# Kernel tuning notes

Hardware: AMD Instinct MI355X
Metric: run time of the kernel (lower is better)

The kernel has to match this reference:

```python
import jax, jax.numpy as jnp
import numpy as np

N_LOC, N_EVT, E = 100000, 200000, 1000000
F_LOC, F_EVT, H = 128, 128, 64


def setup_inputs() -> dict:
    key = jax.random.key(0)
    ks = jax.random.split(key, 12)
    s = lambda k, shp: jax.random.normal(k, shp, dtype=jnp.float32) * (1.0 / np.sqrt(shp[0]))
    return {
        "loc_x": jax.random.normal(ks[0], (N_LOC, F_LOC), dtype=jnp.float32),
        "evt_x": jax.random.normal(ks[1], (N_EVT, F_EVT), dtype=jnp.float32),
        "edge_index": jax.random.randint(ks[2], (2, E), 0, N_LOC, dtype=jnp.int64),
        # projections (stored as (in, out))
        "W_loc": s(ks[3], (F_LOC, H)), "b_loc": jnp.zeros((H,), jnp.float32),
        "W_evt": s(ks[4], (F_EVT, H)), "b_evt": jnp.zeros((H,), jnp.float32),
        # SAGEConv: lin_l (on aggregated src, with bias), lin_r (on dst root, no bias)
        "W_l": s(ks[5], (H, H)), "b_l": jnp.zeros((H,), jnp.float32),
        "W_r": s(ks[6], (H, H)),
        # head MLP
        "W_h1": s(ks[7], (H, H // 2)), "b_h1": jnp.zeros((H // 2,), jnp.float32),
        "W_h2": s(ks[8], (H // 2, 1)), "b_h2": jnp.zeros((1,), jnp.float32),
    }


def reference(loc_x, evt_x, edge_index, W_loc, b_loc, W_evt, b_evt,
              W_l, b_l, W_r, W_h1, b_h1, W_h2, b_h2):
    # node projections + ReLU
    loc_h = jax.nn.relu(loc_x @ W_loc + b_loc)   # [N_loc, H]
    evt_h = jax.nn.relu(evt_x @ W_evt + b_evt)   # [N_evt, H]

    src, dst = edge_index[0], edge_index[1]      # event -> location
    n_loc = loc_h.shape[0]
    # mean aggregation of source (event) features onto destination (location) nodes
    msg_sum = jax.ops.segment_sum(evt_h[src], dst, num_segments=n_loc)   # [N_loc, H]
    cnt = jax.ops.segment_sum(jnp.ones_like(dst, dtype=loc_h.dtype), dst,
                              num_segments=n_loc)
    agg = msg_sum / jnp.maximum(cnt, 1.0)[:, None]
    # SAGEConv: lin_l(agg) + lin_r(root), then ReLU
    loc_h = jax.nn.relu(agg @ W_l + b_l + loc_h @ W_r)

    # prediction head
    h = jax.nn.relu(loc_h @ W_h1 + b_h1)
    logits = (h @ W_h2 + b_h2)[:, 0]             # [N_loc]
    return logits
```

## Files before the change

### kernel.cpp

```cpp
#include <hip/hip_runtime.h>


#define N_LOC 100000
#define N_EVT 200000
#define E_CNT 1000000
#define NTILES 6250
#define NBKT   256
#define BKT_L  391
#define CAPG   6000
#define QCAP   32
#define BKT_BLK 512
#define PERB   1954

#define PROJ_EVT_BLK 512
#define PROJ_LOC_BLK 256
#define PROJ_BLK_TOT (PROJ_EVT_BLK + PROJ_LOC_BLK)
#define EVT_TILES 12500
#define LOC_TILES 6250
#define HEAD_BLK  512

typedef __attribute__((ext_vector_type(8))) short short8;
typedef __attribute__((ext_vector_type(4))) float floatx4;

__device__ __forceinline__ float b2f(unsigned short u) {
    unsigned int x = ((unsigned int)u) << 16;
    return __builtin_bit_cast(float, x);
}
__device__ __forceinline__ unsigned short f2b(float f) {
    unsigned int x = __builtin_bit_cast(unsigned int, f);
    unsigned int r = (x + 0x7fffu + ((x >> 16) & 1u)) >> 16;
    return (unsigned short)r;
}
__device__ __forceinline__ float loadf(const void* p, int f32, size_t i) {
    return f32 ? ((const float*)p)[i] : b2f(((const unsigned short*)p)[i]);
}

__global__ __launch_bounds__(256) void prep_kernel(
    const void* t0, const void* t1, const int* eidx,
    const void* t3, const void* t4, const void* t5, const void* t6,
    const void* t7, const void* t8, const void* t9, const void* t10,
    const void* t11, const void* t12, const void* t13,
    int* flags, int* gbc, unsigned short* __restrict__ wp_all) {
    int b = blockIdx.x, tid = threadIdx.x;
    __shared__ int s0, s1;

    if (b == 14) { gbc[tid] = 0; return; }

    if (b >= 15) {
        int pb = b - 15;
        const void* W; int K, N, bstart, off;
        if (pb < 4)       { W = t5;  K = 128; N = 64; bstart = 0;  off = 0; }
        else if (pb < 8)  { W = t3;  K = 128; N = 64; bstart = 4;  off = 8192; }
        else if (pb < 10) { W = t7;  K = 64;  N = 64; bstart = 8;  off = 16384; }
        else if (pb < 12) { W = t9;  K = 64;  N = 64; bstart = 10; off = 20480; }
        else              { W = t10; K = 64;  N = 32; bstart = 12; off = 24576; }
        if (tid == 0) s0 = 0;
        __syncthreads();
        int nsamp = 2 * K * N; if (nsamp > 1024) nsamp = 1024;
        const unsigned short* h = (const unsigned short*)W;
        int susp = 0;
        for (int i = tid; i < nsamp; i += 256)
            if (((h[i] >> 7) & 0xFF) >= 0x90) susp++;
        if (susp) atomicAdd(&s0, susp);
        __syncthreads();
        int f32 = (s0 * 16 >= nsamp) ? 1 : 0;

        int idx  = (pb - bstart) * 256 + tid;
        int nk   = K >> 5;
        int f    = idx >> 6;
        int lane = idx & 63;
        int t  = f / nk;
        int kk = f - t * nk;
        int n  = t * 16 + (lane & 15);
        int k0 = kk * 32 + (lane >> 4) * 8;
        unsigned short tmp[8];
#pragma unroll
        for (int j = 0; j < 8; ++j) {
            size_t src = (size_t)(k0 + j) * N + n;
            tmp[j] = f32 ? f2b(((const float*)W)[src])
                         : ((const unsigned short*)W)[src];
        }
#pragma unroll
        for (int j = 0; j < 8; ++j) wp_all[(size_t)off + (size_t)idx * 8 + j] = tmp[j];
        return;
    }

    if (tid == 0) { s0 = 0; s1 = 0; }
    __syncthreads();
    if (b == 13) {
        if (tid < 128) {
            if (eidx[2 * tid] != 0) atomicAdd(&s0, 1);
            if (eidx[2 * tid + 1] != 0) atomicAdd(&s1, 1);
        }
        __syncthreads();
        if (tid == 0) flags[2] = (s1 == 0 && s0 > 32) ? 1 : 0;
        return;
    }
    const void* ptrs[13] = {t0, t1, t3, t4, t5, t6, t7, t8, t9, t10, t11, t12, t13};
    const int   cnts[13] = {12800000, 25600000, 8192, 64, 8192, 64,
                            4096, 64, 4096, 2048, 32, 32, 1};
    const int   slot[13] = {0, 1, 3, 4, 5, 6, 7, 8, 9, 10, 11, 12, 13};
    int nsamp = 2 * cnts[b];
    if (nsamp > 1024) nsamp = 1024;
    const unsigned short* h = (const unsigned short*)ptrs[b];
    int susp = 0;
    for (int i = tid; i < nsamp; i += 256)
        if (((h[i] >> 7) & 0xFF) >= 0x90) susp++;
    if (susp) atomicAdd(&s0, susp);
    __syncthreads();
    if (tid == 0) flags[slot[b]] = (s0 * 16 >= nsamp) ? 1 : 0;
}

__global__ __launch_bounds__(256, 3) void proj_both_kernel(
    const void* __restrict__ evt_x, const void* __restrict__ loc_x,
    const unsigned short* __restrict__ wp_all,
    const void* __restrict__ b_evt, const void* __restrict__ b_loc,
    unsigned short* __restrict__ evt_h, unsigned short* __restrict__ loc_h,
    const int* __restrict__ flags) {
    __shared__ unsigned short bs[8192];
    int blk = blockIdx.x;
    int tid = threadIdx.x, lane = tid & 63, wv = tid >> 6;
    int l15 = lane & 15, quad = lane >> 4;

    const void* X; const unsigned short* Wp; const void* bias;
    unsigned short* Y; int fx, fb, w0, nw, ntile;
    if (blk < PROJ_EVT_BLK) {
        X = evt_x; Wp = wp_all;        bias = b_evt; Y = evt_h;
        fx = flags[1]; fb = flags[6];
        w0 = blk * 4 + wv; nw = PROJ_EVT_BLK * 4; ntile = EVT_TILES;
    } else {
        X = loc_x; Wp = wp_all + 8192; bias = b_loc; Y = loc_h;
        fx = flags[0]; fb = flags[4];
        w0 = (blk - PROJ_EVT_BLK) * 4 + wv; nw = PROJ_LOC_BLK * 4; ntile = LOC_TILES;
    }

    {
        const short8* src = reinterpret_cast<const short8*>(Wp);
        short8* dst = reinterpret_cast<short8*>(bs);
#pragma unroll
        for (int i = 0; i < 4; ++i) dst[tid + i * 256] = src[tid + i * 256];
    }
    __syncthreads();

    float bv[4];
#pragma unroll
    for (int q = 0; q < 4; ++q) bv[q] = loadf(bias, fb, q * 16 + l15);

    if (w0 >= ntile) return;

    auto mfma_store = [&](const short8* a, int t) {
        floatx4 acc[4];
#pragma unroll
        for (int q = 0; q < 4; ++q) acc[q] = (floatx4)0.0f;
#pragma unroll
        for (int q = 0; q < 4; ++q) {
            short8 bq[4];
#pragma unroll
            for (int kk = 0; kk < 4; ++kk)
                bq[kk] = *reinterpret_cast<const short8*>(
                    &bs[((q * 4 + kk) * 64 + lane) * 8]);
#pragma unroll
            for (int kk = 0; kk < 4; ++kk)
                acc[q] = __builtin_amdgcn_mfma_f32_16x16x32_bf16(
                    a[kk], bq[kk], acc[q], 0, 0, 0);
        }
#pragma unroll
        for (int q = 0; q < 4; ++q)
#pragma unroll
            for (int r = 0; r < 4; ++r) {
                float v = acc[q][r] + bv[q];
                v = v > 0.0f ? v : 0.0f;
                Y[(size_t)(t * 16 + quad * 4 + r) * 64 + q * 16 + l15] = f2b(v);
            }
    };

    if (fx) {
        const float* Xf = (const float*)X;
        float4 pf[8];
        auto issueF = [&](int t) {
            const float* xr = Xf + (size_t)(t * 16 + l15) * 128 + quad * 8;
#pragma unroll
            for (int kk = 0; kk < 4; ++kk) {
                pf[kk * 2]     = *reinterpret_cast<const float4*>(xr + kk * 32);
                pf[kk * 2 + 1] = *reinterpret_cast<const float4*>(xr + kk * 32 + 4);
            }
        };
        issueF(w0);
        for (int t = w0; t < ntile; t += nw) {
            short8 a[4];
#pragma unroll
            for (int kk = 0; kk < 4; ++kk) {
                float4 p0 = pf[kk * 2], p1 = pf[kk * 2 + 1];
                short8 v;
                v[0] = (short)f2b(p0.x); v[1] = (short)f2b(p0.y);
                v[2] = (short)f2b(p0.z); v[3] = (short)f2b(p0.w);
                v[4] = (short)f2b(p1.x); v[5] = (short)f2b(p1.y);
                v[6] = (short)f2b(p1.z); v[7] = (short)f2b(p1.w);
                a[kk] = v;
            }
            int tn = t + nw;
            if (tn < ntile) issueF(tn);
            mfma_store(a, t);
        }
    } else {
        const unsigned short* Xh = (const unsigned short*)X;
        short8 an[4];
        auto issueH = [&](int t) {
            const unsigned short* xr = Xh + (size_t)(t * 16 + l15) * 128 + quad * 8;
#pragma unroll
            for (int kk = 0; kk < 4; ++kk)
                an[kk] = *reinterpret_cast<const short8*>(xr + kk * 32);
        };
        issueH(w0);
        for (int t = w0; t < ntile; t += nw) {
            short8 a[4];
#pragma unroll
            for (int kk = 0; kk < 4; ++kk) a[kk] = an[kk];
            int tn = t + nw;
            if (tn < ntile) issueH(tn);
            mfma_store(a, t);
        }
    }
}

__global__ __launch_bounds__(256) void bucket_kernel(
    const int* __restrict__ eidx, uint2* __restrict__ bkt,
    int* __restrict__ gbc, const int* __restrict__ flags) {
    __shared__ uint2 queue[NBKT][QCAP];
    __shared__ int qcnt[NBKT];
    int tid = threadIdx.x, blk = blockIdx.x;
    qcnt[tid] = 0;
    __syncthreads();
    int f64 = flags[2];
    const long long* e64 = (const long long*)eidx;
    int e0 = blk * PERB;
    int e1 = e0 + PERB; if (e1 > E_CNT) e1 = E_CNT;
    const int rounds = (PERB + 255) / 256;

    for (int r = 0; r < rounds; ++r) {
        int e = e0 + r * 256 + tid;
        if (e < e1) {
            int src, dst;
            if (f64) { src = (int)e64[e]; dst = (int)e64[E_CNT + e]; }
            else     { src = eidx[e];     dst = eidx[E_CNT + e]; }
            if ((unsigned)dst < (unsigned)N_LOC && (unsigned)src < (unsigned)N_EVT) {
                int bk = dst / BKT_L;
                int pos = atomicAdd(&qcnt[bk], 1);
                if (pos < QCAP) {
                    queue[bk][pos] = make_uint2((unsigned)src, (unsigned)dst);
                } else {
                    int p = atomicAdd(&gbc[bk], 1);
                    if (p < CAPG) bkt[(size_t)bk * CAPG + p] = make_uint2(src, dst);
                }
            }
        }
        __syncthreads();
        int n = qcnt[tid]; if (n > QCAP) n = QCAP;
        while (n >= 16) {
            int gp = atomicAdd(&gbc[tid], 16);
            if (gp + 16 <= CAPG) {
                uint2* d = bkt + (size_t)tid * CAPG + gp;
#pragma unroll
                for (int j = 0; j < 16; ++j) d[j] = queue[tid][j];
            }
#pragma unroll
            for (int j = 16; j < QCAP; ++j) queue[tid][j - 16] = queue[tid][j];
            n -= 16;
        }
        qcnt[tid] = n;
        __syncthreads();
    }
    int n = qcnt[tid]; if (n > QCAP) n = QCAP;
    if (n > 0) {
        int gp = atomicAdd(&gbc[tid], n);
        for (int j = 0; j < n; ++j)
            if (gp + j < CAPG) bkt[(size_t)tid * CAPG + gp + j] = queue[tid][j];
    }
}

__global__ void scan_gbc_kernel(const int* __restrict__ gbc,
                                int* __restrict__ bbase) {
    __shared__ int sh[256];
    int t = threadIdx.x;
    int v = gbc[t]; if (v > CAPG) v = CAPG;
    sh[t] = v;
    __syncthreads();
    for (int d = 1; d < 256; d <<= 1) {
        int x = (t >= d) ? sh[t - d] : 0;
        __syncthreads();
        sh[t] += x;
        __syncthreads();
    }
    bbase[t] = sh[t] - v;
}

__global__ __launch_bounds__(256) void csr_build_kernel(
    const uint2* __restrict__ bkt, const int* __restrict__ gbc,
    const int* __restrict__ bbase,
    int* __restrict__ rowptr, int* __restrict__ csr) {
    __shared__ int lcnt[512];
    __shared__ int lscan[512];
    __shared__ int lcsr[CAPG];
    int b = blockIdx.x, tid = threadIdx.x;
    int loc0 = b * BKT_L;
    int nloc = N_LOC - loc0; if (nloc > BKT_L) nloc = BKT_L;
    int cntE = gbc[b]; if (cntE > CAPG) cntE = CAPG;
    int base = bbase[b];
    const uint2* bp = bkt + (size_t)b * CAPG;

    int i0 = tid, i1 = tid + 256;
    lcnt[i0] = 0; lcnt[i1] = 0;
    __syncthreads();
    for (int i = tid; i < cntE; i += 256) {
        int d = (int)bp[i].y - loc0;
        atomicAdd(&lcnt[d], 1);
    }
    __syncthreads();
    lscan[i0] = lcnt[i0]; lscan[i1] = lcnt[i1];
    __syncthreads();
    for (int d = 1; d < 512; d <<= 1) {
        int v0 = (i0 >= d) ? lscan[i0 - d] : 0;
        int v1 = (i1 >= d) ? lscan[i1 - d] : 0;
        __syncthreads();
        lscan[i0] += v0; lscan[i1] += v1;
        __syncthreads();
    }
    for (int i = tid; i < nloc; i += 256) {
        int excl = lscan[i] - lcnt[i];
        rowptr[loc0 + i] = base + excl;
        lcnt[i] = excl;
    }
    if (b == NBKT - 1 && tid == 0) rowptr[N_LOC] = base + cntE;
    __syncthreads();
    for (int i = tid; i < cntE; i += 256) {
        uint2 pr = bp[i];
        int d = (int)pr.y - loc0;
        int p = atomicAdd(&lcnt[d], 1);
        if (p < CAPG) lcsr[p] = (int)pr.x;
    }
    __syncthreads();
    for (int i = tid; i < cntE; i += 256) csr[base + i] = lcsr[i];
}

__global__ __launch_bounds__(256) void aggregate_kernel(
    const unsigned short* __restrict__ evt_h,
    const int* __restrict__ rowptr, const int* __restrict__ csr,
    unsigned short* __restrict__ agg, int N) {
    int wid  = (blockIdx.x * 256 + threadIdx.x) >> 6;
    int lane = threadIdx.x & 63;
    if (wid >= N) return;
    int e0 = rowptr[wid], e1 = rowptr[wid + 1];
    float acc = 0.0f;
    for (int j = e0; j < e1; j += 4) {
        int c1 = j + 1 < e1, c2 = j + 2 < e1, c3 = j + 3 < e1;
        int s0 = csr[j];
        int s1 = csr[c1 ? j + 1 : j];
        int s2 = csr[c2 ? j + 2 : j];
        int s3 = csr[c3 ? j + 3 : j];
        float v0 = b2f(evt_h[(size_t)s0 * 64 + lane]);
        float v1 = b2f(evt_h[(size_t)s1 * 64 + lane]);
        float v2 = b2f(evt_h[(size_t)s2 * 64 + lane]);
        float v3 = b2f(evt_h[(size_t)s3 * 64 + lane]);
        acc += v0;
        if (c1) acc += v1;
        if (c2) acc += v2;
        if (c3) acc += v3;
    }
    float inv = (e1 > e0) ? 1.0f / (float)(e1 - e0) : 0.0f;
    agg[(size_t)wid * 64 + lane] = f2b(acc * inv);
}

__global__ __launch_bounds__(256, 3) void head_kernel(
    const unsigned short* __restrict__ agg,
    const unsigned short* __restrict__ loc_h,
    const unsigned short* __restrict__ wp_all,
    const void* __restrict__ bl, const void* __restrict__ bh1,
    const void* __restrict__ wh2, const void* __restrict__ bh2,
    void* __restrict__ out, const int* __restrict__ flags) {
    __shared__ unsigned short bls[4096];
    __shared__ unsigned short brs[4096];
    __shared__ unsigned short b1s[2048];
    __shared__ unsigned short h2s[4][16 * 64];
    int tid = threadIdx.x, lane = tid & 63, wv = tid >> 6;
    int l15 = lane & 15, quad = lane >> 4;
    int fbl = flags[8], fbh1 = flags[11], fwh2 = flags[12], fbh2 = flags[13];
    int fout = flags[0];
    const unsigned short* wp_l  = wp_all + 16384;
    const unsigned short* wp_r  = wp_all + 20480;
    const unsigned short* wp_h1 = wp_all + 24576;

    {
        const short8* sl = reinterpret_cast<const short8*>(wp_l);
        const short8* sr = reinterpret_cast<const short8*>(wp_r);
        const short8* s1 = reinterpret_cast<const short8*>(wp_h1);
        short8* dl = reinterpret_cast<short8*>(bls);
        short8* dr = reinterpret_cast<short8*>(brs);
        short8* d1 = reinterpret_cast<short8*>(b1s);
        dl[tid] = sl[tid]; dl[tid + 256] = sl[tid + 256];
        dr[tid] = sr[tid]; dr[tid + 256] = sr[tid + 256];
        d1[tid] = s1[tid];
    }
    __syncthreads();

    float bbl[4], bh1v[2], w2v[2];
#pragma unroll
    for (int q = 0; q < 4; ++q) bbl[q] = loadf(bl, fbl, q * 16 + l15);
#pragma unroll
    for (int q = 0; q < 2; ++q) {
        bh1v[q] = loadf(bh1, fbh1, q * 16 + l15);
        w2v[q]  = loadf(wh2, fwh2, q * 16 + l15);
    }
    float bb2 = loadf(bh2, fbh2, 0);

    const int NW = HEAD_BLK * 4;
    int w0 = blockIdx.x * 4 + wv;
    if (w0 >= NTILES) return;

    short8 c0[4], c1[4];

    auto issue = [&](short8* c, int t) {
        int m = t * 16 + l15;
#pragma unroll
        for (int kk = 0; kk < 2; ++kk) {
            c[kk]     = *reinterpret_cast<const short8*>(
                agg + (size_t)m * 64 + kk * 32 + quad * 8);
            c[2 + kk] = *reinterpret_cast<const short8*>(
                loc_h + (size_t)m * 64 + kk * 32 + quad * 8);
        }
    };

    auto compute = [&](const short8* c, int tile) {
        floatx4 acc[4];
#pragma unroll
        for (int q = 0; q < 4; ++q) acc[q] = (floatx4)0.0f;
#pragma unroll
        for (int q = 0; q < 4; ++q) {
            short8 bwl[2], bwr[2];
#pragma unroll
            for (int kk = 0; kk < 2; ++kk) {
                bwl[kk] = *reinterpret_cast<const short8*>(
                    &bls[((q * 2 + kk) * 64 + lane) * 8]);
                bwr[kk] = *reinterpret_cast<const short8*>(
                    &brs[((q * 2 + kk) * 64 + lane) * 8]);
            }
#pragma unroll
            for (int kk = 0; kk < 2; ++kk) {
                acc[q] = __builtin_amdgcn_mfma_f32_16x16x32_bf16(
                    c[kk], bwl[kk], acc[q], 0, 0, 0);
                acc[q] = __builtin_amdgcn_mfma_f32_16x16x32_bf16(
                    c[2 + kk], bwr[kk], acc[q], 0, 0, 0);
            }
        }
#pragma unroll
        for (int q = 0; q < 4; ++q)
#pragma unroll
            for (int r = 0; r < 4; ++r) {
                float v = acc[q][r] + bbl[q];
                v = v > 0.0f ? v : 0.0f;
                h2s[wv][(quad * 4 + r) * 64 + q * 16 + l15] = f2b(v);
            }
        short8 aH[2];
#pragma unroll
        for (int kk = 0; kk < 2; ++kk)
            aH[kk] = *reinterpret_cast<const short8*>(
                &h2s[wv][l15 * 64 + kk * 32 + quad * 8]);

        floatx4 a1[2];
#pragma unroll
        for (int q = 0; q < 2; ++q) a1[q] = (floatx4)0.0f;
#pragma unroll
        for (int q = 0; q < 2; ++q) {
            short8 bw1[2];
#pragma unroll
            for (int kk = 0; kk < 2; ++kk)
                bw1[kk] = *reinterpret_cast<const short8*>(
                    &b1s[((q * 2 + kk) * 64 + lane) * 8]);
#pragma unroll
            for (int kk = 0; kk < 2; ++kk)
                a1[q] = __builtin_amdgcn_mfma_f32_16x16x32_bf16(
                    aH[kk], bw1[kk], a1[q], 0, 0, 0);
        }

        float s[4] = {0.f, 0.f, 0.f, 0.f};
#pragma unroll
        for (int q = 0; q < 2; ++q)
#pragma unroll
            for (int r = 0; r < 4; ++r) {
                float v = a1[q][r] + bh1v[q];
                v = v > 0.0f ? v : 0.0f;
                s[r] += v * w2v[q];
            }
#pragma unroll
        for (int r = 0; r < 4; ++r) {
            s[r] += __shfl_xor(s[r], 1);
            s[r] += __shfl_xor(s[r], 2);
            s[r] += __shfl_xor(s[r], 4);
            s[r] += __shfl_xor(s[r], 8);
        }
#pragma unroll
        for (int r = 0; r < 4; ++r) {
            if (l15 == r) {
                int row = tile * 16 + quad * 4 + r;
                float v = s[r] + bb2;
                if (fout) ((float*)out)[row] = v;
                else      ((unsigned short*)out)[row] = f2b(v);
            }
        }
    };

    issue(c0, w0);
    int t = w0;
    while (true) {
        int tn = t + NW;
        bool hn = tn < NTILES;
        if (hn) issue(c1, tn);
        compute(c0, t);
        if (!hn) break;
        t = tn; tn = t + NW; hn = tn < NTILES;
        if (hn) issue(c0, tn);
        compute(c1, t);
        if (!hn) break;
        t = tn;
    }
}

extern "C" void kernel_launch(void* const* d_in, const int* in_sizes, int n_in,
                              void* d_out, int out_size, void* d_ws, size_t ws_size,
                              hipStream_t stream) {
    (void)in_sizes; (void)n_in; (void)out_size; (void)ws_size;
    const void* loc_x = d_in[0];
    const void* evt_x = d_in[1];
    const int*  eidx  = (const int*)d_in[2];
    const void* W_loc = d_in[3];
    const void* b_loc = d_in[4];
    const void* W_evt = d_in[5];
    const void* b_evt = d_in[6];
    const void* W_l   = d_in[7];
    const void* b_l   = d_in[8];
    const void* W_r   = d_in[9];
    const void* W_h1  = d_in[10];
    const void* b_h1  = d_in[11];
    const void* W_h2  = d_in[12];
    const void* b_h2  = d_in[13];

    char* ws = (char*)d_ws;
    unsigned short* evt_h  = (unsigned short*)(ws);
    unsigned short* loc_h  = (unsigned short*)(ws + 25600000);
    int*            csr    = (int*)(ws + 38400000);
    int*            rowptr = (int*)(ws + 42400000);
    int*            gbc    = (int*)(ws + 42800016);
    int*            bbase  = (int*)(ws + 42801040);
    unsigned short* wp_all = (unsigned short*)(ws + 42802064);
    int*            flags  = (int*)(ws + 42855312);
    uint2*          bkt    = (uint2*)(ws + 42855376);
    unsigned short* agg    = (unsigned short*)(ws + 42855376);

    prep_kernel<<<28, 256, 0, stream>>>(
        loc_x, evt_x, eidx, W_loc, b_loc, W_evt, b_evt,
        W_l, b_l, W_r, W_h1, b_h1, W_h2, b_h2,
        flags, gbc, wp_all);

    proj_both_kernel<<<PROJ_BLK_TOT, 256, 0, stream>>>(
        evt_x, loc_x, wp_all, b_evt, b_loc, evt_h, loc_h, flags);

    bucket_kernel<<<BKT_BLK, 256, 0, stream>>>(eidx, bkt, gbc, flags);
    scan_gbc_kernel<<<1, 256, 0, stream>>>(gbc, bbase);
    csr_build_kernel<<<NBKT, 256, 0, stream>>>(bkt, gbc, bbase, rowptr, csr);

    aggregate_kernel<<<(N_LOC + 3) / 4, 256, 0, stream>>>(evt_h, rowptr, csr,
                                                          agg, N_LOC);

    head_kernel<<<HEAD_BLK, 256, 0, stream>>>(
        agg, loc_h, wp_all, b_l, b_h1, W_h2, b_h2, d_out, flags);
}
```

Baseline: 317.5 us.

## Vectorize aggregation gathers, fold bucket scan into CSR build, double projection grid

The aggregate kernel now has each wave handle 8 edges at once, with every lane loading 8 bf16 values (16 bytes) of a source row. Partial sums are combined with xor shuffles. This replaces per-lane 2-byte gathers with wider loads and should raise memory efficiency on the random-access gather. The separate single-block scan kernel is removed, and each CSR-build block now recomputes the 256-entry prefix scan redundantly, saving one launch. The projection grid is doubled and its launch bound raised to 4 waves per SIMD, which may constrain registers.

```diff
diff --git a/kernel.cpp b/kernel.cpp
--- a/kernel.cpp
+++ b/kernel.cpp
@@ -12,8 +12,8 @@
 #define BKT_BLK 512
 #define PERB   1954
 
-#define PROJ_EVT_BLK 512
-#define PROJ_LOC_BLK 256
+#define PROJ_EVT_BLK 1024
+#define PROJ_LOC_BLK 512
 #define PROJ_BLK_TOT (PROJ_EVT_BLK + PROJ_LOC_BLK)
 #define EVT_TILES 12500
 #define LOC_TILES 6250
@@ -21,6 +21,8 @@
 
 typedef __attribute__((ext_vector_type(8))) short short8;
 typedef __attribute__((ext_vector_type(4))) float floatx4;
+typedef __attribute__((ext_vector_type(4))) unsigned short ushort4v;
+typedef __attribute__((ext_vector_type(8))) unsigned short ushort8v;
 
 __device__ __forceinline__ float b2f(unsigned short u) {
     unsigned int x = ((unsigned int)u) << 16;
@@ -111,7 +113,7 @@
     if (tid == 0) flags[slot[b]] = (s0 * 16 >= nsamp) ? 1 : 0;
 }
 
-__global__ __launch_bounds__(256, 3) void proj_both_kernel(
+__global__ __launch_bounds__(256, 4) void proj_both_kernel(
     const void* __restrict__ evt_x, const void* __restrict__ loc_x,
     const unsigned short* __restrict__ wp_all,
     const void* __restrict__ b_evt, const void* __restrict__ b_loc,
@@ -278,34 +280,28 @@
     }
 }
 
-__global__ void scan_gbc_kernel(const int* __restrict__ gbc,
-                                int* __restrict__ bbase) {
-    __shared__ int sh[256];
-    int t = threadIdx.x;
-    int v = gbc[t]; if (v > CAPG) v = CAPG;
-    sh[t] = v;
-    __syncthreads();
-    for (int d = 1; d < 256; d <<= 1) {
-        int x = (t >= d) ? sh[t - d] : 0;
-        __syncthreads();
-        sh[t] += x;
-        __syncthreads();
-    }
-    bbase[t] = sh[t] - v;
-}
-
 __global__ __launch_bounds__(256) void csr_build_kernel(
     const uint2* __restrict__ bkt, const int* __restrict__ gbc,
-    const int* __restrict__ bbase,
     int* __restrict__ rowptr, int* __restrict__ csr) {
+    __shared__ int sg[256];
     __shared__ int lcnt[512];
     __shared__ int lscan[512];
     __shared__ int lcsr[CAPG];
     int b = blockIdx.x, tid = threadIdx.x;
     int loc0 = b * BKT_L;
     int nloc = N_LOC - loc0; if (nloc > BKT_L) nloc = BKT_L;
+
+    int gv = gbc[tid]; if (gv > CAPG) gv = CAPG;
+    sg[tid] = gv;
+    __syncthreads();
+    for (int d = 1; d < 256; d <<= 1) {
+        int x = (tid >= d) ? sg[tid - d] : 0;
+        __syncthreads();
+        sg[tid] += x;
+        __syncthreads();
+    }
     int cntE = gbc[b]; if (cntE > CAPG) cntE = CAPG;
-    int base = bbase[b];
+    int base = sg[b] - cntE;
     const uint2* bp = bkt + (size_t)b * CAPG;
 
     int i0 = tid, i1 = tid + 256;
@@ -348,26 +344,48 @@
     unsigned short* __restrict__ agg, int N) {
     int wid  = (blockIdx.x * 256 + threadIdx.x) >> 6;
     int lane = threadIdx.x & 63;
+    int eo = lane >> 3, cg = lane & 7;
     if (wid >= N) return;
     int e0 = rowptr[wid], e1 = rowptr[wid + 1];
-    float acc = 0.0f;
-    for (int j = e0; j < e1; j += 4) {
-        int c1 = j + 1 < e1, c2 = j + 2 < e1, c3 = j + 3 < e1;
-        int s0 = csr[j];
-        int s1 = csr[c1 ? j + 1 : j];
-        int s2 = csr[c2 ? j + 2 : j];
-        int s3 = csr[c3 ? j + 3 : j];
-        float v0 = b2f(evt_h[(size_t)s0 * 64 + lane]);
-        float v1 = b2f(evt_h[(size_t)s1 * 64 + lane]);
-        float v2 = b2f(evt_h[(size_t)s2 * 64 + lane]);
-        float v3 = b2f(evt_h[(size_t)s3 * 64 + lane]);
-        acc += v0;
-        if (c1) acc += v1;
-        if (c2) acc += v2;
-        if (c3) acc += v3;
+    float a[8];
+#pragma unroll
+    for (int k = 0; k < 8; ++k) a[k] = 0.0f;
+
+    int j = e0;
+    for (; j + 16 <= e1; j += 16) {
+        int s0 = csr[j + eo];
+        int s1 = csr[j + 8 + eo];
+        ushort8v v0 = *reinterpret_cast<const ushort8v*>(
+            evt_h + (size_t)s0 * 64 + cg * 8);
+        ushort8v v1 = *reinterpret_cast<const ushort8v*>(
+            evt_h + (size_t)s1 * 64 + cg * 8);
+#pragma unroll
+        for (int k = 0; k < 8; ++k) a[k] += b2f(v0[k]) + b2f(v1[k]);
+    }
+    for (; j < e1; j += 8) {
+        int jj = j + eo;
+        bool c = jj < e1;
+        int s = csr[c ? jj : j];
+        ushort8v v = *reinterpret_cast<const ushort8v*>(
+            evt_h + (size_t)s * 64 + cg * 8);
+        if (c) {
+#pragma unroll
+            for (int k = 0; k < 8; ++k) a[k] += b2f(v[k]);
+        }
+    }
+#pragma unroll
+    for (int k = 0; k < 8; ++k) {
+        a[k] += __shfl_xor(a[k], 8);
+        a[k] += __shfl_xor(a[k], 16);
+        a[k] += __shfl_xor(a[k], 32);
     }
     float inv = (e1 > e0) ? 1.0f / (float)(e1 - e0) : 0.0f;
-    agg[(size_t)wid * 64 + lane] = f2b(acc * inv);
+    if (eo == 0) {
+        ushort8v o;
+#pragma unroll
+        for (int k = 0; k < 8; ++k) o[k] = f2b(a[k] * inv);
+        *reinterpret_cast<ushort8v*>(agg + (size_t)wid * 64 + cg * 8) = o;
+    }
 }
 
 __global__ __launch_bounds__(256, 3) void head_kernel(
@@ -549,7 +567,6 @@
     int*            csr    = (int*)(ws + 38400000);
     int*            rowptr = (int*)(ws + 42400000);
     int*            gbc    = (int*)(ws + 42800016);
-    int*            bbase  = (int*)(ws + 42801040);
     unsigned short* wp_all = (unsigned short*)(ws + 42802064);
     int*            flags  = (int*)(ws + 42855312);
     uint2*          bkt    = (uint2*)(ws + 42855376);
@@ -564,8 +581,7 @@
         evt_x, loc_x, wp_all, b_evt, b_loc, evt_h, loc_h, flags);
 
     bucket_kernel<<<BKT_BLK, 256, 0, stream>>>(eidx, bkt, gbc, flags);
-    scan_gbc_kernel<<<1, 256, 0, stream>>>(gbc, bbase);
-    csr_build_kernel<<<NBKT, 256, 0, stream>>>(bkt, gbc, bbase, rowptr, csr);
+    csr_build_kernel<<<NBKT, 256, 0, stream>>>(bkt, gbc, rowptr, csr);
 
     aggregate_kernel<<<(N_LOC + 3) / 4, 256, 0, stream>>>(evt_h, rowptr, csr,
                                                           agg, N_LOC);
```

Result: slower. 328.4 us (+3.4%).
